# Kernel optimization log

Measured on AMD Instinct MI355X. Metric: run time of the kernel, lower is better.

Reference implementation:

```python
import jax, jax.numpy as jnp
import numpy as np

GAMMA = 0.1
PENALTY = 0.0
BANDWIDTH = 1.0e6
B, N, M = 64, 512, 512


def setup_inputs() -> dict:
    key = jax.random.key(0)
    k1, k2, k3 = jax.random.split(key, 3)
    D = jax.random.uniform(k1, (B, N, M), dtype=jnp.float32)
    mask = jnp.ones((B, N, M), dtype=jnp.float32)
    # valid lengths in [N/2, N] so R[b, x_lens[b], y_lens[b]] is always reachable
    x_lens = jax.random.randint(k2, (B,), N // 2, N + 1)
    y_lens = jax.random.randint(k3, (B,), M // 2, M + 1)
    return {"D": D, "mask": mask, "x_lens": x_lens, "y_lens": y_lens}


def _softdtw(D, x_lens, y_lens):
    # Soft-DTW DP over anti-diagonals. D: [B, N, M] masked cost.
    # Returns per-batch loss R[b, x_lens[b], y_lens[b]].
    Bn, Nn, Mn = D.shape
    inv_gamma = 1.0 / GAMMA
    inf = jnp.float32(jnp.inf)
    ii = jnp.arange(Nn + 1)  # row index i = 0..N within a diagonal buffer
    im1 = jnp.clip(ii - 1, 0, Nn)
    # diagonal buffers: entry i of diag s holds R[i, s - i]
    d0 = jnp.full((Bn, Nn + 1), inf).at[:, 0].set(0.0)  # s=0: only R[0,0]=0
    d1 = jnp.full((Bn, Nn + 1), inf)                    # s=1: boundary, all inf
    xl = x_lens[:, None]
    yl = y_lens[:, None]

    def step(carry, s):
        dm2, dm1 = carry                      # diagonals s-2 and s-1
        jj = s - ii                           # column index j for each i
        r00 = dm2[:, im1]                     # R[i-1, j-1]
        r01 = dm1[:, im1]                     # R[i-1, j]
        r10 = dm1                             # R[i,   j-1]
        r0 = -r00 * inv_gamma
        r1 = -(r01 + PENALTY) * inv_gamma
        r2 = -(r10 + PENALTY) * inv_gamma
        rmax = jnp.maximum(jnp.maximum(r0, r1), r2)
        finite = jnp.isfinite(rmax)
        rs = jnp.where(finite, rmax, 0.0)     # safe max (avoid inf-inf -> nan)
        rsum = jnp.exp(r0 - rs) + jnp.exp(r1 - rs) + jnp.exp(r2 - rs)
        softmin = jnp.where(finite, -GAMMA * (jnp.log(rsum) + rs), inf)
        dcell = D[:, jnp.clip(ii - 1, 0, Nn - 1), jnp.clip(jj - 1, 0, Mn - 1)]
        new = dcell + softmin                 # R[i, j] = D[i-1, j-1] + softmin
        valid = (ii >= 1) & (ii <= Nn) & (jj >= 1) & (jj <= Mn)
        valid = valid & (jnp.abs(jj - ii) <= BANDWIDTH)
        upd = valid[None, :] & (ii[None, :] <= xl) & (jj[None, :] <= yl)
        dnew = jnp.where(upd, new, inf)
        return (dm1, dnew), dnew

    _, diags = jax.lax.scan(step, (d0, d1), jnp.arange(2, Nn + Mn + 1))
    # diags: [N+M-1, B, N+1]; diag index s-2 holds cells with i+j == s
    s_idx = jnp.clip(x_lens + y_lens - 2, 0, Nn + Mn - 2)
    loss = diags[s_idx, jnp.arange(Bn), x_lens]
    return loss


def reference(D, mask, x_lens, y_lens):
    return _softdtw(D * mask, x_lens, y_lens)
```

## Files before the change

kernel.cpp:

```cpp
#include <hip/hip_runtime.h>


constexpr int Bn = 64, Nn = 512, Mn = 512;
constexpr int TARGET_E = -30;

__device__ __forceinline__ float exp2_fast(float x) {
    float r; asm("v_exp_f32 %0, %1" : "=v"(r) : "v"(x)); return r;
}
__device__ __forceinline__ float log2_fast(float x) {
    float r; asm("v_log_f32 %0, %1" : "=v"(r) : "v"(x)); return r;
}
__device__ __forceinline__ float ldexp_fast(float x, int e) {
    float r; asm("v_ldexp_f32 %0, %1, %2" : "=v"(r) : "v"(x), "v"(e)); return r;
}
__device__ __forceinline__ int frexp_exp(float x) {
    int r; asm("v_frexp_exp_i32_f32 %0, %1" : "=v"(r) : "v"(x)); return r;
}

__device__ __forceinline__ int shup1_i(int x, bool sel) {
    int a = __builtin_amdgcn_update_dpp(x, x, 0x111, 0xf, 0xf, false);
    int b = __builtin_amdgcn_update_dpp(x, x, 0x142, 0xf, 0xf, false);
    return sel ? b : a;
}
__device__ __forceinline__ float shup1_f(float x, bool sel) {
    return __int_as_float(shup1_i(__float_as_int(x), sel));
}

#define PLOAD(MM, BD, BM)                                                      \
    {   const int base_ = 4 * ((MM) - t);                                      \
        _Pragma("unroll")                                                      \
        for (int rr = 0; rr < 4; ++rr) {                                       \
            int r_ = min(max(base_ + rr, 0), Nn - 1);                          \
            int o_ = r_ * (Mn / 4) + chunk;                                    \
            BD[rr][0] = D4[o_];  BD[rr][1] = D4[o_ + 1];                       \
            BM[rr][0] = M4[o_];  BM[rr][1] = M4[o_ + 1];                       \
        } }

#define PBUILD(MM, BD, BM)                                                     \
    {   const int s_ = (MM) % 6;                                               \
        _Pragma("unroll")                                                      \
        for (int rr = 0; rr < 4; ++rr) {                                       \
            float4 p_ = BD[rr][0] * BM[rr][0] * negk;                          \
            float4 q_ = BD[rr][1] * BM[rr][1] * negk;                          \
            float4 wa_, wb_;                                                   \
            wa_.x = exp2_fast(p_.x);  wa_.y = exp2_fast(p_.y);                 \
            wa_.z = exp2_fast(p_.z);  wa_.w = exp2_fast(p_.w);                 \
            wb_.x = exp2_fast(q_.x);  wb_.y = exp2_fast(q_.y);                 \
            wb_.z = exp2_fast(q_.z);  wb_.w = exp2_fast(q_.w);                 \
            wlds[s_][2 * rr][t]     = wa_;                                     \
            wlds[s_][2 * rr + 1][t] = wb_;                                     \
        } }

#define CSTEP(MM, WCUR, WNXT)                                                  \
    {                                                                          \
        const int m_ = (MM);                                                   \
        if (m_ <= 63) {                                                        \
            if (m_ == t && t != 0) {                                           \
                _Pragma("unroll")                                              \
                for (int c = 0; c < 8; ++c) E[c] = 0.0f;                       \
                Ld = 0.0f;                                                     \
            }                                                                  \
        }                                                                      \
        float ce3_, co_[4];                                                    \
        _Pragma("unroll")                                                      \
        for (int rr = 0; rr < 4; ++rr) {                                       \
            const float Wr_[8] = {                                             \
                WCUR[rr][0].x, WCUR[rr][0].y, WCUR[rr][0].z, WCUR[rr][0].w,    \
                WCUR[rr][1].x, WCUR[rr][1].y, WCUR[rr][1].z, WCUR[rr][1].w };  \
            const float c0s_ = (rr == 0) ? Ld : L[rr - 1];                     \
            float c2_ = L[rr];                                                 \
            float A_[8], Bv_[8];                                               \
            A_[0] = E[0] + c0s_;                                               \
            _Pragma("unroll")                                                  \
            for (int c = 1; c < 8; ++c) A_[c] = E[c] + E[c - 1];               \
            _Pragma("unroll")                                                  \
            for (int c = 0; c < 8; ++c) Bv_[c] = Wr_[c] * A_[c];               \
            _Pragma("unroll")                                                  \
            for (int c = 0; c < 8; ++c) {                                      \
                float nv_ = fmaf(Wr_[c], c2_, Bv_[c]);                         \
                E[c] = nv_;  c2_ = nv_;                                        \
            }                                                                  \
            if (rr == 3) ce3_ = c2_;                                           \
            co_[rr] = shup1_f(c2_, selrow);                                    \
            if (m_ == m_out && rr == r_out) {         \
                float sel_ = E[0];                                             \
                if (c_out == 1) sel_ = E[1];  if (c_out == 2) sel_ = E[2];     \
                if (c_out == 3) sel_ = E[3];  if (c_out == 4) sel_ = E[4];     \
                if (c_out == 5) sel_ = E[5];  if (c_out == 6) sel_ = E[6];     \
                if (c_out == 7) sel_ = E[7];                                   \
                ov = sel_;  ovS = S;                                           \
            }                                                                  \
        }                                                                      \
        int So_ = shup1_i(S, selrow);                                          \
        int eo_ = frexp_exp(ce3_);                                             \
        int ei_ = frexp_exp(co_[3]) + (So_ - S);                               \
        bool own0_  = (ce3_ == 0.0f);                                          \
        bool incok_ = (t != 0) && (co_[3] != 0.0f);                            \
        int  eref_  = (incok_ && ((ei_ > eo_) || own0_)) ? ei_ : eo_;          \
        int  shift_ = (own0_ && !incok_) ? 0 : (TARGET_E - eref_);             \
        if (m_ < t) shift_ = S - So_;                \
        int Snew_ = S - shift_;                                                \
        _Pragma("unroll")                                                      \
        for (int c = 0; c < 8; ++c) E[c] = ldexp_fast(E[c], shift_);           \
        Ld = ldexp_fast(L[3], shift_);                                         \
        {   int d_ = So_ - Snew_;                                              \
            _Pragma("unroll")                                                  \
            for (int rr = 0; rr < 4; ++rr)                                     \
                L[rr] = (t == 0) ? 0.0f : ldexp_fast(co_[rr], d_);             \
        }                                                                      \
        S = Snew_;                                                             \
        {   const int sn_ = (m_ + 1) % 6;       \
            _Pragma("unroll")                                                  \
            for (int rr = 0; rr < 4; ++rr) {                                   \
                WNXT[rr][0] = wlds[sn_][2 * rr][t];                            \
                WNXT[rr][1] = wlds[sn_][2 * rr + 1][t];                        \
            } }                                                                \
    }

__global__ __launch_bounds__(192) void softdtw_fwd(
    const float* __restrict__ D, const float* __restrict__ Msk,
    const int* __restrict__ xlens, const int* __restrict__ ylens,
    float* __restrict__ out)
{
    const int tid = threadIdx.x;
    const int w   = tid >> 6;
    const int t   = tid & 63;
    const bool selrow = ((t & 15) == 0);
    const int b   = blockIdx.x;
    const int xl = xlens[b];
    const int yl = ylens[b];
    const int t_out = (yl - 1) >> 3;
    const int c_out = (yl - 1) & 7;
    const int r_out = (xl - 1) & 3;
    const int m_out = ((xl - 1) >> 2) + t_out;
    const int nsuper = (m_out >> 1) + 1;

    const float negk = -14.4269504088896341f;
    const float klog = 0.06931471805599453f;

    __shared__ float4 wlds[6][8][64];

    const float4* __restrict__ D4 = (const float4*)(D   + (size_t)b * (Nn * Mn));
    const float4* __restrict__ M4 = (const float4*)(Msk + (size_t)b * (Nn * Mn));
    const int chunk = t * 2;

    float E[8];
#pragma unroll
    for (int c = 0; c < 8; ++c) E[c] = 0.0f;
    float L[4] = {0.0f, 0.0f, 0.0f, 0.0f};
    float Ld = (t == 0) ? 1.0f : 0.0f;
    int S = 0;
    float ov = 1.0f;  int ovS = 0;
    float4 Wc[4][2], Wn[4][2];

    const int p = w - 1;
    float4 bD0[4][2], bM0[4][2], bD1[4][2], bM1[4][2];

    if (w != 0) {
        PLOAD(p, bD0, bM0);      PBUILD(p, bD0, bM0);
        PLOAD(p + 2, bD0, bM0);  PBUILD(p + 2, bD0, bM0);
        PLOAD(4 + p, bD1, bM1);
    }
    __syncthreads();

    if (w == 0) {
#pragma unroll
        for (int rr = 0; rr < 4; ++rr) {
            Wc[rr][0] = wlds[0][2 * rr][t];
            Wc[rr][1] = wlds[0][2 * rr + 1][t];
        }
    }

    for (int u = 0; u < nsuper; ++u) {
        if (w == 0) {
            CSTEP(2 * u, Wc, Wn);
            if (2 * u + 1 <= m_out) CSTEP(2 * u + 1, Wn, Wc);
        } else {
            if (u & 1) { PLOAD(2 * u + 6 + p, bD1, bM1);
                         PBUILD(2 * u + 4 + p, bD0, bM0); }
            else       { PLOAD(2 * u + 6 + p, bD0, bM0);
                         PBUILD(2 * u + 4 + p, bD1, bM1); }
        }
        __syncthreads();
    }

    if (w == 0 && t == t_out) {
        int   ev = frexp_exp(ov);
        float mv = ldexp_fast(ov, -ev);
        out[b] = -(log2_fast(mv) + (float)(ev + ovS)) * klog;
    }
}

extern "C" void kernel_launch(void* const* d_in, const int* in_sizes, int n_in,
                              void* d_out, int out_size, void* d_ws, size_t ws_size,
                              hipStream_t stream) {
    const float* D   = (const float*)d_in[0];
    const float* Msk = (const float*)d_in[1];
    const int*   xl  = (const int*)d_in[2];
    const int*   yl  = (const int*)d_in[3];
    float* out = (float*)d_out;
    softdtw_fwd<<<dim3(Bn), dim3(192), 0, stream>>>(D, Msk, xl, yl, out);
}
```

Measured before the change: 161.1 us.

## Interleave two batches per single wavefront and drop LDS producer warps

The kernel now runs one 64-thread wavefront per block. That wavefront processes two batch elements with interleaved DP steps. It replaces the earlier scheme, where two producer wavefronts built exp weights into LDS and synchronised with a compute wavefront. Loads and exp are software-pipelined in registers, and the two independent recurrences hide each other's latency. The change removes the per-step __syncthreads and the LDS traffic, but it halves the grid to 32 blocks, raises register pressure, and runs each pair until the longer of the two lengths.

```diff
diff --git a/kernel.cpp b/kernel.cpp
--- a/kernel.cpp
+++ b/kernel.cpp
@@ -26,34 +26,36 @@
     return __int_as_float(shup1_i(__float_as_int(x), sel));
 }
 
-#define PLOAD(MM, BD, BM)                                                      \
+#define PLOAD(MM, bD, bM, D4p, M4p)                                            \
     {   const int base_ = 4 * ((MM) - t);                                      \
         _Pragma("unroll")                                                      \
         for (int rr = 0; rr < 4; ++rr) {                                       \
             int r_ = min(max(base_ + rr, 0), Nn - 1);                          \
             int o_ = r_ * (Mn / 4) + chunk;                                    \
-            BD[rr][0] = D4[o_];  BD[rr][1] = D4[o_ + 1];                       \
-            BM[rr][0] = M4[o_];  BM[rr][1] = M4[o_ + 1];                       \
+            bD[rr][0] = D4p[o_];  bD[rr][1] = D4p[o_ + 1];                     \
+            bM[rr][0] = M4p[o_];  bM[rr][1] = M4p[o_ + 1];                     \
         } }
 
-#define PBUILD(MM, BD, BM)                                                     \
-    {   const int s_ = (MM) % 6;                                               \
-        _Pragma("unroll")                                                      \
+#define PMUL(PR, bD, bM)                                                       \
+    {   _Pragma("unroll")                                                      \
         for (int rr = 0; rr < 4; ++rr) {                                       \
-            float4 p_ = BD[rr][0] * BM[rr][0] * negk;                          \
-            float4 q_ = BD[rr][1] * BM[rr][1] * negk;                          \
-            float4 wa_, wb_;                                                   \
-            wa_.x = exp2_fast(p_.x);  wa_.y = exp2_fast(p_.y);                 \
-            wa_.z = exp2_fast(p_.z);  wa_.w = exp2_fast(p_.w);                 \
-            wb_.x = exp2_fast(q_.x);  wb_.y = exp2_fast(q_.y);                 \
-            wb_.z = exp2_fast(q_.z);  wb_.w = exp2_fast(q_.w);                 \
-            wlds[s_][2 * rr][t]     = wa_;                                     \
-            wlds[s_][2 * rr + 1][t] = wb_;                                     \
+            float4 p_ = bD[rr][0] * bM[rr][0] * negk;                          \
+            float4 q_ = bD[rr][1] * bM[rr][1] * negk;                          \
+            PR[rr * 8 + 0] = p_.x;  PR[rr * 8 + 1] = p_.y;                     \
+            PR[rr * 8 + 2] = p_.z;  PR[rr * 8 + 3] = p_.w;                     \
+            PR[rr * 8 + 4] = q_.x;  PR[rr * 8 + 5] = q_.y;                     \
+            PR[rr * 8 + 6] = q_.z;  PR[rr * 8 + 7] = q_.w;                     \
         } }
 
-#define CSTEP(MM, WCUR, WNXT)                                                  \
+#define WBUILD(W, PR)                                                          \
+    {   _Pragma("unroll")                                                      \
+        for (int ii_ = 0; ii_ < 32; ++ii_) W[ii_] = exp2_fast(PR[ii_]);        }
+
+#define STEP(MM, E, L, Ld, S, ov, ovS, W, PR, bD, bM, D4p, M4p,                \
+             TOUT, COUT, ROUT, MOUT)                                           \
     {                                                                          \
         const int m_ = (MM);                                                   \
+        PLOAD(m_ + 2, bD, bM, D4p, M4p);                                       \
         if (m_ <= 63) {                                                        \
             if (m_ == t && t != 0) {                                           \
                 _Pragma("unroll")                                              \
@@ -64,9 +66,6 @@
         float ce3_, co_[4];                                                    \
         _Pragma("unroll")                                                      \
         for (int rr = 0; rr < 4; ++rr) {                                       \
-            const float Wr_[8] = {                                             \
-                WCUR[rr][0].x, WCUR[rr][0].y, WCUR[rr][0].z, WCUR[rr][0].w,    \
-                WCUR[rr][1].x, WCUR[rr][1].y, WCUR[rr][1].z, WCUR[rr][1].w };  \
             const float c0s_ = (rr == 0) ? Ld : L[rr - 1];                     \
             float c2_ = L[rr];                                                 \
             float A_[8], Bv_[8];                                               \
@@ -74,20 +73,20 @@
             _Pragma("unroll")                                                  \
             for (int c = 1; c < 8; ++c) A_[c] = E[c] + E[c - 1];               \
             _Pragma("unroll")                                                  \
-            for (int c = 0; c < 8; ++c) Bv_[c] = Wr_[c] * A_[c];               \
+            for (int c = 0; c < 8; ++c) Bv_[c] = W[rr * 8 + c] * A_[c];        \
             _Pragma("unroll")                                                  \
             for (int c = 0; c < 8; ++c) {                                      \
-                float nv_ = fmaf(Wr_[c], c2_, Bv_[c]);                         \
+                float nv_ = fmaf(W[rr * 8 + c], c2_, Bv_[c]);                  \
                 E[c] = nv_;  c2_ = nv_;                                        \
             }                                                                  \
             if (rr == 3) ce3_ = c2_;                                           \
             co_[rr] = shup1_f(c2_, selrow);                                    \
-            if (m_ == m_out && rr == r_out) {         \
+            if (m_ == (MOUT) && rr == (ROUT)) {       \
                 float sel_ = E[0];                                             \
-                if (c_out == 1) sel_ = E[1];  if (c_out == 2) sel_ = E[2];     \
-                if (c_out == 3) sel_ = E[3];  if (c_out == 4) sel_ = E[4];     \
-                if (c_out == 5) sel_ = E[5];  if (c_out == 6) sel_ = E[6];     \
-                if (c_out == 7) sel_ = E[7];                                   \
+                if ((COUT) == 1) sel_ = E[1];  if ((COUT) == 2) sel_ = E[2];   \
+                if ((COUT) == 3) sel_ = E[3];  if ((COUT) == 4) sel_ = E[4];   \
+                if ((COUT) == 5) sel_ = E[5];  if ((COUT) == 6) sel_ = E[6];   \
+                if ((COUT) == 7) sel_ = E[7];                                  \
                 ov = sel_;  ovS = S;                                           \
             }                                                                  \
         }                                                                      \
@@ -109,85 +108,74 @@
                 L[rr] = (t == 0) ? 0.0f : ldexp_fast(co_[rr], d_);             \
         }                                                                      \
         S = Snew_;                                                             \
-        {   const int sn_ = (m_ + 1) % 6;       \
-            _Pragma("unroll")                                                  \
-            for (int rr = 0; rr < 4; ++rr) {                                   \
-                WNXT[rr][0] = wlds[sn_][2 * rr][t];                            \
-                WNXT[rr][1] = wlds[sn_][2 * rr + 1][t];                        \
-            } }                                                                \
+        WBUILD(W, PR);                                     \
+        PMUL(PR, bD, bM);                               \
     }
 
-__global__ __launch_bounds__(192) void softdtw_fwd(
+__global__ __launch_bounds__(64) void softdtw_fwd(
     const float* __restrict__ D, const float* __restrict__ Msk,
     const int* __restrict__ xlens, const int* __restrict__ ylens,
     float* __restrict__ out)
 {
-    const int tid = threadIdx.x;
-    const int w   = tid >> 6;
-    const int t   = tid & 63;
+    const int t = threadIdx.x;
     const bool selrow = ((t & 15) == 0);
-    const int b   = blockIdx.x;
-    const int xl = xlens[b];
-    const int yl = ylens[b];
-    const int t_out = (yl - 1) >> 3;
-    const int c_out = (yl - 1) & 7;
-    const int r_out = (xl - 1) & 3;
-    const int m_out = ((xl - 1) >> 2) + t_out;
-    const int nsuper = (m_out >> 1) + 1;
+    const int b0 = 2 * blockIdx.x;
+    const int b1 = 2 * blockIdx.x + 1;
+
+    const int xl0 = xlens[b0], yl0 = ylens[b0];
+    const int xl1 = xlens[b1], yl1 = ylens[b1];
+    const int t_out0 = (yl0 - 1) >> 3, c_out0 = (yl0 - 1) & 7;
+    const int r_out0 = (xl0 - 1) & 3,  m_out0 = ((xl0 - 1) >> 2) + t_out0;
+    const int t_out1 = (yl1 - 1) >> 3, c_out1 = (yl1 - 1) & 7;
+    const int r_out1 = (xl1 - 1) & 3,  m_out1 = ((xl1 - 1) >> 2) + t_out1;
+    const int mmax = max(m_out0, m_out1);
 
     const float negk = -14.4269504088896341f;
     const float klog = 0.06931471805599453f;
 
-    __shared__ float4 wlds[6][8][64];
-
-    const float4* __restrict__ D4 = (const float4*)(D   + (size_t)b * (Nn * Mn));
-    const float4* __restrict__ M4 = (const float4*)(Msk + (size_t)b * (Nn * Mn));
+    const float4* __restrict__ D40 = (const float4*)(D   + (size_t)b0 * (Nn * Mn));
+    const float4* __restrict__ M40 = (const float4*)(Msk + (size_t)b0 * (Nn * Mn));
+    const float4* __restrict__ D41 = (const float4*)(D   + (size_t)b1 * (Nn * Mn));
+    const float4* __restrict__ M41 = (const float4*)(Msk + (size_t)b1 * (Nn * Mn));
     const int chunk = t * 2;
 
-    float E[8];
+    float E0[8];  float L0[4] = {0, 0, 0, 0};
 #pragma unroll
-    for (int c = 0; c < 8; ++c) E[c] = 0.0f;
-    float L[4] = {0.0f, 0.0f, 0.0f, 0.0f};
-    float Ld = (t == 0) ? 1.0f : 0.0f;
-    int S = 0;
-    float ov = 1.0f;  int ovS = 0;
-    float4 Wc[4][2], Wn[4][2];
+    for (int c = 0; c < 8; ++c) E0[c] = 0.0f;
+    float Ld0 = (t == 0) ? 1.0f : 0.0f;
+    int S0 = 0;  float ov0 = 1.0f;  int ovS0 = 0;
+    float W0[32], PR0[32];
+    float4 bD0[4][2], bM0[4][2];
 
-    const int p = w - 1;
-    float4 bD0[4][2], bM0[4][2], bD1[4][2], bM1[4][2];
+    float E1[8];  float L1[4] = {0, 0, 0, 0};
+#pragma unroll
+    for (int c = 0; c < 8; ++c) E1[c] = 0.0f;
+    float Ld1 = (t == 0) ? 1.0f : 0.0f;
+    int S1 = 0;  float ov1 = 1.0f;  int ovS1 = 0;
+    float W1[32], PR1[32];
+    float4 bD1[4][2], bM1[4][2];
 
-    if (w != 0) {
-        PLOAD(p, bD0, bM0);      PBUILD(p, bD0, bM0);
-        PLOAD(p + 2, bD0, bM0);  PBUILD(p + 2, bD0, bM0);
-        PLOAD(4 + p, bD1, bM1);
-    }
-    __syncthreads();
+    PLOAD(0, bD0, bM0, D40, M40);  PMUL(PR0, bD0, bM0);  WBUILD(W0, PR0);
+    PLOAD(1, bD0, bM0, D40, M40);  PMUL(PR0, bD0, bM0);
+    PLOAD(0, bD1, bM1, D41, M41);  PMUL(PR1, bD1, bM1);  WBUILD(W1, PR1);
+    PLOAD(1, bD1, bM1, D41, M41);  PMUL(PR1, bD1, bM1);
 
-    if (w == 0) {
-#pragma unroll
-        for (int rr = 0; rr < 4; ++rr) {
-            Wc[rr][0] = wlds[0][2 * rr][t];
-            Wc[rr][1] = wlds[0][2 * rr + 1][t];
-        }
+    for (int m = 0; m <= mmax; ++m) {
+        STEP(m, E0, L0, Ld0, S0, ov0, ovS0, W0, PR0, bD0, bM0, D40, M40,
+             t_out0, c_out0, r_out0, m_out0);
+        STEP(m, E1, L1, Ld1, S1, ov1, ovS1, W1, PR1, bD1, bM1, D41, M41,
+             t_out1, c_out1, r_out1, m_out1);
     }
 
-    for (int u = 0; u < nsuper; ++u) {
-        if (w == 0) {
-            CSTEP(2 * u, Wc, Wn);
-            if (2 * u + 1 <= m_out) CSTEP(2 * u + 1, Wn, Wc);
-        } else {
-            if (u & 1) { PLOAD(2 * u + 6 + p, bD1, bM1);
-                         PBUILD(2 * u + 4 + p, bD0, bM0); }
-            else       { PLOAD(2 * u + 6 + p, bD0, bM0);
-                         PBUILD(2 * u + 4 + p, bD1, bM1); }
-        }
-        __syncthreads();
+    if (t == t_out0) {
+        int   ev = frexp_exp(ov0);
+        float mv = ldexp_fast(ov0, -ev);
+        out[b0] = -(log2_fast(mv) + (float)(ev + ovS0)) * klog;
     }
-
-    if (w == 0 && t == t_out) {
-        int   ev = frexp_exp(ov);
-        float mv = ldexp_fast(ov, -ev);
-        out[b] = -(log2_fast(mv) + (float)(ev + ovS)) * klog;
+    if (t == t_out1) {
+        int   ev = frexp_exp(ov1);
+        float mv = ldexp_fast(ov1, -ev);
+        out[b1] = -(log2_fast(mv) + (float)(ev + ovS1)) * klog;
     }
 }
 
@@ -199,5 +187,5 @@
     const int*   xl  = (const int*)d_in[2];
     const int*   yl  = (const int*)d_in[3];
     float* out = (float*)d_out;
-    softdtw_fwd<<<dim3(Bn), dim3(192), 0, stream>>>(D, Msk, xl, yl, out);
+    softdtw_fwd<<<dim3(Bn / 2), dim3(64), 0, stream>>>(D, Msk, xl, yl, out);
 }
```

After: 327.2 us. 103% more time.

## Spread producer loads across eight waves, one row each, and prioritize compute wave

Applied to the files above, without the earlier changes.

The block grows from 3 to 9 wavefronts. Each producer wave now loads and exponentiates a single row of the 4-row slab for its slot instead of all four rows, which spreads the global-load latency and exp work across more waves and cuts per-wave register buffers. The compute wave also raises its scheduling priority with s_setprio so the serial DP wave is favored over the producers. The cost is more waves joining each block barrier, and higher per-block resource use.

```diff
diff --git a/kernel.cpp b/kernel.cpp
--- a/kernel.cpp
+++ b/kernel.cpp
@@ -26,30 +26,26 @@
     return __int_as_float(shup1_i(__float_as_int(x), sel));
 }
 
-#define PLOAD(MM, BD, BM)                                                      \
-    {   const int base_ = 4 * ((MM) - t);                                      \
-        _Pragma("unroll")                                                      \
-        for (int rr = 0; rr < 4; ++rr) {                                       \
-            int r_ = min(max(base_ + rr, 0), Nn - 1);                          \
-            int o_ = r_ * (Mn / 4) + chunk;                                    \
-            BD[rr][0] = D4[o_];  BD[rr][1] = D4[o_ + 1];                       \
-            BM[rr][0] = M4[o_];  BM[rr][1] = M4[o_ + 1];                       \
-        } }
-
-#define PBUILD(MM, BD, BM)                                                     \
-    {   const int s_ = (MM) % 6;                                               \
-        _Pragma("unroll")                                                      \
-        for (int rr = 0; rr < 4; ++rr) {                                       \
-            float4 p_ = BD[rr][0] * BM[rr][0] * negk;                          \
-            float4 q_ = BD[rr][1] * BM[rr][1] * negk;                          \
-            float4 wa_, wb_;                                                   \
-            wa_.x = exp2_fast(p_.x);  wa_.y = exp2_fast(p_.y);                 \
-            wa_.z = exp2_fast(p_.z);  wa_.w = exp2_fast(p_.w);                 \
-            wb_.x = exp2_fast(q_.x);  wb_.y = exp2_fast(q_.y);                 \
-            wb_.z = exp2_fast(q_.z);  wb_.w = exp2_fast(q_.w);                 \
-            wlds[s_][2 * rr][t]     = wa_;                                     \
-            wlds[s_][2 * rr + 1][t] = wb_;                                     \
-        } }
+#define PLOAD1(SLOT, RB, BD, BM)                                               \
+    {   int r0_ = 4 * ((SLOT) - t) + (RB);                                     \
+        int r_  = min(max(r0_, 0), Nn - 1);                                    \
+        int o_  = r_ * (Mn / 4) + chunk;                                       \
+        BD[0] = D4[o_];  BD[1] = D4[o_ + 1];                                   \
+        BM[0] = M4[o_];  BM[1] = M4[o_ + 1];                                   \
+    }
+
+#define PBUILD1(SLOT, RB, BD, BM)                                              \
+    {   const int s_ = (SLOT) % 6;                                             \
+        float4 p_ = BD[0] * BM[0] * negk;                                      \
+        float4 q_ = BD[1] * BM[1] * negk;                                      \
+        float4 wa_, wb_;                                                       \
+        wa_.x = exp2_fast(p_.x);  wa_.y = exp2_fast(p_.y);                     \
+        wa_.z = exp2_fast(p_.z);  wa_.w = exp2_fast(p_.w);                     \
+        wb_.x = exp2_fast(q_.x);  wb_.y = exp2_fast(q_.y);                     \
+        wb_.z = exp2_fast(q_.z);  wb_.w = exp2_fast(q_.w);                     \
+        wlds[s_][2 * (RB)][t]     = wa_;                                       \
+        wlds[s_][2 * (RB) + 1][t] = wb_;                                       \
+    }
 
 #define CSTEP(MM, WCUR, WNXT)                                                  \
     {                                                                          \
@@ -117,7 +113,7 @@
             } }                                                                \
     }
 
-__global__ __launch_bounds__(192) void softdtw_fwd(
+__global__ __launch_bounds__(576) void softdtw_fwd(
     const float* __restrict__ D, const float* __restrict__ Msk,
     const int* __restrict__ xlens, const int* __restrict__ ylens,
     float* __restrict__ out)
@@ -153,13 +149,17 @@
     float ov = 1.0f;  int ovS = 0;
     float4 Wc[4][2], Wn[4][2];
 
-    const int p = w - 1;
-    float4 bD0[4][2], bM0[4][2], bD1[4][2], bM1[4][2];
-
-    if (w != 0) {
-        PLOAD(p, bD0, bM0);      PBUILD(p, bD0, bM0);
-        PLOAD(p + 2, bD0, bM0);  PBUILD(p + 2, bD0, bM0);
-        PLOAD(4 + p, bD1, bM1);
+    const int q  = w - 1;
+    const int qs = q >> 2;
+    const int qr = q & 3;
+    float4 bD0[2], bM0[2], bD1[2], bM1[2];
+
+    if (w == 0) {
+        __builtin_amdgcn_s_setprio(1);
+    } else {
+        PLOAD1(qs, qr, bD0, bM0);      PBUILD1(qs, qr, bD0, bM0);
+        PLOAD1(2 + qs, qr, bD0, bM0);  PBUILD1(2 + qs, qr, bD0, bM0);
+        PLOAD1(4 + qs, qr, bD1, bM1);
     }
     __syncthreads();
 
@@ -176,10 +176,10 @@
             CSTEP(2 * u, Wc, Wn);
             if (2 * u + 1 <= m_out) CSTEP(2 * u + 1, Wn, Wc);
         } else {
-            if (u & 1) { PLOAD(2 * u + 6 + p, bD1, bM1);
-                         PBUILD(2 * u + 4 + p, bD0, bM0); }
-            else       { PLOAD(2 * u + 6 + p, bD0, bM0);
-                         PBUILD(2 * u + 4 + p, bD1, bM1); }
+            if (u & 1) { PLOAD1(2 * u + 6 + qs, qr, bD1, bM1);
+                         PBUILD1(2 * u + 4 + qs, qr, bD0, bM0); }
+            else       { PLOAD1(2 * u + 6 + qs, qr, bD0, bM0);
+                         PBUILD1(2 * u + 4 + qs, qr, bD1, bM1); }
         }
         __syncthreads();
     }
@@ -199,5 +199,5 @@
     const int*   xl  = (const int*)d_in[2];
     const int*   yl  = (const int*)d_in[3];
     float* out = (float*)d_out;
-    softdtw_fwd<<<dim3(Bn), dim3(192), 0, stream>>>(D, Msk, xl, yl, out);
-}
+    softdtw_fwd<<<dim3(Bn), dim3(576), 0, stream>>>(D, Msk, xl, yl, out);
+}
```

After: 175.4 us. 8.9% more time.
